# Kernel tuning notes

Hardware: AMD Instinct MI355X
Metric: run time of the kernel (lower is better)

Reference implementation:

```python
import jax, jax.numpy as jnp
import numpy as np

B, T, C, E = 2, 100, 80, 32
MH = MW = 64
IN_H = IN_W = 640.0
IOU_FACTOR, CLS_FACTOR, TOPK = 6.0, 0.5, 10
EPS = 1e-9


def get_anchors_and_scalers(fmaps, in_h, in_w):
    anchors, scalers = [], []
    for fh, fw in fmaps:
        stride = in_h / fh
        ys = (np.arange(fh) + 0.5) * stride
        xs = (np.arange(fw) + 0.5) * stride
        gy, gx = np.meshgrid(ys, xs, indexing='ij')
        anchors.append(np.stack([gx, gy], -1).reshape(-1, 2))
        scalers.append(np.full(fh * fw, stride))
    return (np.concatenate(anchors).astype(np.float32),
            np.concatenate(scalers).astype(np.float32))


def setup_inputs() -> dict:
    key = jax.random.key(0)
    ks = jax.random.split(key, 8)
    anchors_np, scalers_np = get_anchors_and_scalers([(80, 80), (40, 40), (20, 20)], IN_H, IN_W)
    anchors = jnp.asarray(anchors_np)
    scalers = jnp.asarray(scalers_np)
    A = anchors.shape[0]
    cls_logits = jax.random.normal(ks[0], (B, A, C), jnp.float32)
    wh = jax.random.uniform(ks[1], (B, A, 2), jnp.float32, 16.0, 160.0)
    ctr = anchors[None] + jax.random.normal(ks[2], (B, A, 2), jnp.float32) * 8.0
    pred_boxes = jnp.clip(jnp.concatenate([ctr - wh / 2, ctr + wh / 2], -1), 0.0, IN_W)
    mask_embs = jax.random.normal(ks[3], (B, A, E), jnp.float32)
    protos = jax.random.normal(ks[4], (B, MH, MW, E), jnp.float32)
    tl = jax.random.uniform(ks[5], (B, T, 2), jnp.float32, 0.0, 560.0)
    twh = jax.random.uniform(ks[6], (B, T, 2), jnp.float32, 30.0, 240.0)
    target_bbox = jnp.concatenate([tl, jnp.minimum(tl + twh, IN_W)], -1)
    target_cls = jax.random.randint(ks[7], (B, T), 0, C, jnp.int32)
    target_masks = (jax.random.uniform(jax.random.fold_in(key, 7), (B, MH, MW, T)) > 0.5).astype(jnp.float32)
    return {'cls_logits': cls_logits, 'pred_boxes': pred_boxes, 'mask_embs': mask_embs,
            'protos': protos, 'target_cls': target_cls, 'target_bbox': target_bbox,
            'target_masks': target_masks, 'anchors': anchors, 'scalers': scalers}


def _ciou_pairwise(gt, pr):
    # gt [B,T,4], pr [B,A,4] -> [B,T,A]
    g = gt[:, :, None, :]
    p = pr[:, None, :, :]
    ix1 = jnp.maximum(g[..., 0], p[..., 0]); iy1 = jnp.maximum(g[..., 1], p[..., 1])
    ix2 = jnp.minimum(g[..., 2], p[..., 2]); iy2 = jnp.minimum(g[..., 3], p[..., 3])
    inter = jnp.clip(ix2 - ix1, 0.0) * jnp.clip(iy2 - iy1, 0.0)
    wg = g[..., 2] - g[..., 0]; hg = g[..., 3] - g[..., 1]
    wp = p[..., 2] - p[..., 0]; hp = p[..., 3] - p[..., 1]
    union = wg * hg + wp * hp - inter + EPS
    iou = inter / union
    cw = jnp.maximum(g[..., 2], p[..., 2]) - jnp.minimum(g[..., 0], p[..., 0])
    ch = jnp.maximum(g[..., 3], p[..., 3]) - jnp.minimum(g[..., 1], p[..., 1])
    c2 = cw * cw + ch * ch + EPS
    rho2 = ((g[..., 0] + g[..., 2] - p[..., 0] - p[..., 2]) ** 2 +
            (g[..., 1] + g[..., 3] - p[..., 1] - p[..., 3]) ** 2) / 4.0
    v = (4.0 / (jnp.pi ** 2)) * (jnp.arctan(wg / (hg + EPS)) - jnp.arctan(wp / (hp + EPS))) ** 2
    alpha = jax.lax.stop_gradient(v / (1.0 - iou + v + EPS))
    return iou - rho2 / c2 - alpha * v


def _bbox_mask(boxes, mh, mw, in_h, in_w):
    # boxes [B,A,4] pixel xyxy -> [B,A,mh,mw] binary inside-box mask on mask grid
    sx, sy = mw / in_w, mh / in_h
    x1, y1, x2, y2 = boxes[..., 0] * sx, boxes[..., 1] * sy, boxes[..., 2] * sx, boxes[..., 3] * sy
    rows = jnp.arange(mh, dtype=boxes.dtype)
    cols = jnp.arange(mw, dtype=boxes.dtype)
    rm = (rows >= y1[..., None]) & (rows < y2[..., None])  # [B,A,mh]
    cm = (cols >= x1[..., None]) & (cols < x2[..., None])  # [B,A,mw]
    return (rm[..., :, None] & cm[..., None, :]).astype(boxes.dtype)


def _assign_and_build(cls_logits, pred_boxes, mask_embs, protos,
                      target_cls, target_bbox, target_masks, anchors, scalers):
    Bn, A, Cn = cls_logits.shape
    mh, mw = protos.shape[1], protos.shape[2]
    # --- task-aligned assigner ---
    lt, rb = target_bbox[:, :, None, :2], target_bbox[:, :, None, 2:]
    deltas = jnp.concatenate([anchors[None, None] - lt, rb - anchors[None, None]], -1)
    grid_mask = (jnp.min(deltas, -1) > 0).astype(cls_logits.dtype)  # [B,T,A]
    iou_mat = jnp.clip(_ciou_pairwise(target_bbox, pred_boxes), 0.0, 1.0)  # [B,T,A]
    cls_prob = jax.nn.sigmoid(cls_logits)  # [B,A,C]
    oh_t = jax.nn.one_hot(target_cls, Cn, dtype=cls_prob.dtype)  # [B,T,C]
    cls_mat = jnp.einsum('btc,bac->bta', oh_t, cls_prob)  # [B,T,A]
    tmat = grid_mask * (iou_mat ** IOU_FACTOR) * (cls_mat ** CLS_FACTOR)
    kth = jax.lax.top_k(tmat, TOPK)[0][..., -1:]  # [B,T,1]
    topk_targets = jnp.where((tmat >= kth) & (tmat > 0), tmat, 0.0)
    unique_idx = jnp.argmax(topk_targets, axis=1)  # [B,A] best GT per anchor
    valid = (jnp.sum(topk_targets, axis=1) > 0).astype(cls_logits.dtype)  # [B,A]
    align_bbox = jnp.take_along_axis(target_bbox, jnp.broadcast_to(unique_idx[..., None], (Bn, A, 4)), axis=1)
    align_cls_idx = jnp.take_along_axis(target_cls, unique_idx, axis=1)  # [B,A]
    max_target = jnp.max(tmat, axis=-1, keepdims=True)
    max_iou = jnp.max(iou_mat, axis=-1, keepdims=True)
    norm_term = tmat / (max_target + EPS) * max_iou  # [B,T,A]
    norm_g = jnp.take_along_axis(jnp.transpose(norm_term, (0, 2, 1)), unique_idx[..., None], axis=2)  # [B,A,1]
    align_cls = jax.nn.one_hot(align_cls_idx, Cn, dtype=cls_logits.dtype) * norm_g * valid[..., None]
    # --- loss-target assembly (compute_loss body) ---
    align_bbox_scaled = align_bbox / scalers[None, :, None]
    boxes_scaled = pred_boxes / scalers[None, :, None]
    box_target = jnp.concatenate([align_bbox_scaled, valid[..., None], align_cls], -1)
    box_mask = _bbox_mask(align_bbox, mh, mw, IN_H, IN_W)  # [B,A,mh,mw]
    valid_seg = box_mask * valid[..., None, None]
    seg_pred = jax.nn.sigmoid(jnp.einsum('bne,bhwe->bnhw', mask_embs, protos)) * valid_seg
    seg_pred = seg_pred.reshape(Bn, A, mh * mw)
    masks_t = jnp.transpose(target_masks, (0, 3, 1, 2))  # [B,T,mh,mw]
    idx4 = jnp.broadcast_to(unique_idx[..., None, None], (Bn, A, mh, mw))
    align_seg = (jnp.take_along_axis(masks_t, idx4, axis=1) * valid_seg).reshape(Bn, A, mh * mw)
    area = ((align_bbox[..., 2] - align_bbox[..., 0]) * (align_bbox[..., 3] - align_bbox[..., 1])
            / (IN_W * IN_H))
    seg_target = jnp.concatenate([area[..., None], valid[..., None], align_seg], -1)
    return jnp.concatenate([boxes_scaled, cls_logits, box_target, seg_pred, seg_target], -1)


def reference(cls_logits, pred_boxes, mask_embs, protos, target_cls, target_bbox,
              target_masks, anchors, scalers):
    return _assign_and_build(cls_logits, pred_boxes, mask_embs, protos,
                             target_cls, target_bbox, target_masks, anchors, scalers)
```

## Files before the change

kernel.cpp:

```cpp
#include <hip/hip_runtime.h>
#include <math.h>

#define A_TOT 8400
#define B_N   2
#define T_N   100
#define C_N   80
#define E_N   32
#define MH_N  64
#define MW_N  64
#define ROW_N 8363
#define NROWS (B_N*A_TOT)
#define EPSF  1e-9f
#define COMP_CAP 1536
#define NEGINF -1e30f

__device__ __forceinline__ float2 tmat_eval(
    float gx1, float gy1, float gx2, float gy2,
    float ax,  float ay,
    float px1, float py1, float px2, float py2,
    float cl, float atg, float atp) {
  float ix1 = fmaxf(gx1,px1), iy1 = fmaxf(gy1,py1);
  float ix2 = fminf(gx2,px2), iy2 = fminf(gy2,py2);
  float inter = fmaxf(ix2-ix1,0.f) * fmaxf(iy2-iy1,0.f);
  float wg = gx2-gx1, hg = gy2-gy1, wp = px2-px1, hp = py2-py1;
  float uni = wg*hg + wp*hp - inter + EPSF;
  float iou = inter / uni;
  float cw = fmaxf(gx2,px2) - fminf(gx1,px1);
  float ch = fmaxf(gy2,py2) - fminf(gy1,py1);
  float c2 = cw*cw + ch*ch + EPSF;
  float dx = gx1+gx2-px1-px2, dy = gy1+gy2-py1-py2;
  float rho2 = (dx*dx + dy*dy) * 0.25f;
  float da = atg - atp;
  float v  = 0.4052847345693511f * da * da;
  float alpha = v / (1.f - iou + v + EPSF);
  float ciou = iou - rho2/c2 - alpha*v;
  float iouc = fminf(fmaxf(ciou, 0.f), 1.f);

  float tm = 0.f;
  if (ax > gx1 && ay > gy1 && ax < gx2 && ay < gy2) {
    float cp = 1.f / (1.f + expf(-cl));
    float i2 = iouc * iouc;
    tm = i2*i2*i2 * sqrtf(cp);
  }
  return make_float2(tm, iouc);
}

__global__ __launch_bounds__(512) void k_score(
    const float* __restrict__ cls_logits, const float* __restrict__ pred_boxes,
    const float* __restrict__ target_bbox, const int* __restrict__ target_cls,
    const float* __restrict__ anchors,
    float* __restrict__ tmat,
    float* __restrict__ kth, float* __restrict__ maxt, float* __restrict__ maxiou) {
  int bt   = blockIdx.x;
  int b    = bt / T_N;
  int tid  = threadIdx.x;
  int lane = tid & 63, wid = tid >> 6;
  __shared__ float comp[COMP_CAP];
  __shared__ float redm[8], redi[8];
  __shared__ float wtop[8][10];
  __shared__ int   cnt;
  if (tid == 0) cnt = 0;
  __syncthreads();

  float4 g  = *(const float4*)(target_bbox + bt*4);
  int    tc = target_cls[bt];
  float atg = atanf((g.z - g.x) / ((g.w - g.y) + EPSF));
  float* trow = tmat + (size_t)bt * A_TOT;

  float lm = 0.f, li = 0.f;
  for (int a = tid; a < A_TOT; a += 512) {
    float ax = anchors[a*2+0], ay = anchors[a*2+1];
    float4 pb = *(const float4*)(pred_boxes + ((size_t)(b*A_TOT+a))*4);
    float cl = cls_logits[((size_t)(b*A_TOT+a))*C_N + tc];
    float atp = atanf((pb.z - pb.x) / ((pb.w - pb.y) + EPSF));
    float2 r = tmat_eval(g.x,g.y,g.z,g.w, ax,ay, pb.x,pb.y,pb.z,pb.w,
                         cl, atg, atp);
    trow[a] = r.x;
    li = fmaxf(li, r.y);
    if (r.x > 0.f) {
      lm = fmaxf(lm, r.x);
      comp[atomicAdd(&cnt, 1)] = r.x;
    }
  }
  #pragma unroll
  for (int off = 32; off; off >>= 1) {
    lm = fmaxf(lm, __shfl_xor(lm, off));
    li = fmaxf(li, __shfl_xor(li, off));
  }
  if (lane == 0) { redm[wid] = lm; redi[wid] = li; }
  __syncthreads();
  if (tid == 0) {
    float m = redm[0], mi = redi[0];
    #pragma unroll
    for (int w = 1; w < 8; w++) { m = fmaxf(m, redm[w]); mi = fmaxf(mi, redi[w]); }
    maxt[bt] = m; maxiou[bt] = mi;
  }
  int count = cnt;

  int base = wid*64 + lane;
  float e0 = (base        < count) ? comp[base]        : NEGINF;
  float e1 = (base + 512  < count) ? comp[base + 512]  : NEGINF;
  float e2 = (base + 1024 < count) ? comp[base + 1024] : NEGINF;
  float mytop = NEGINF;
  #pragma unroll
  for (int k = 0; k < 10; k++) {
    float bv = e0; int bs = 0;
    if (e1 > bv) { bv = e1; bs = 1; }
    if (e2 > bv) { bv = e2; bs = 2; }
    float v = bv; int id = (lane << 2) | bs;
    #pragma unroll
    for (int off = 32; off; off >>= 1) {
      float ov = __shfl_xor(v, off); int oid = __shfl_xor(id, off);
      if (ov > v || (ov == v && oid < id)) { v = ov; id = oid; }
    }
    if ((id >> 2) == lane) {
      int s = id & 3;
      if (s == 0) e0 = NEGINF; else if (s == 1) e1 = NEGINF; else e2 = NEGINF;
    }
    if (lane == k) mytop = v;
  }
  if (lane < 10) wtop[wid][lane] = mytop;
  __syncthreads();

  if (wid == 0) {
    int ia = lane, ib = 64 + lane;
    float f0 = wtop[ia/10][ia%10];
    float f1 = (ib < 80) ? wtop[ib/10][ib%10] : NEGINF;
    float cur = NEGINF;
    #pragma unroll
    for (int k = 0; k < 10; k++) {
      float bv = f0; int bs = 0;
      if (f1 > bv) { bv = f1; bs = 1; }
      float v = bv; int id = (lane << 1) | bs;
      #pragma unroll
      for (int off = 32; off; off >>= 1) {
        float ov = __shfl_xor(v, off); int oid = __shfl_xor(id, off);
        if (ov > v || (ov == v && oid < id)) { v = ov; id = oid; }
      }
      if ((id >> 1) == lane) { if ((id & 1) == 0) f0 = NEGINF; else f1 = NEGINF; }
      cur = v;
    }
    if (lane == 0) kth[bt] = fmaxf(cur, 0.f);
  }
}

__global__ __launch_bounds__(256) void k_sparse(
    const float* __restrict__ cls_logits, const float* __restrict__ pred_boxes,
    const float* __restrict__ mask_embs,  const float* __restrict__ protos,
    const float* __restrict__ t_masks,    const float* __restrict__ tmat,
    const float* __restrict__ kth, const float* __restrict__ maxt,
    const float* __restrict__ maxiou, const float* __restrict__ target_bbox,
    const int* __restrict__ target_cls, const float* __restrict__ scalers,
    float* __restrict__ out) {
  unsigned row = blockIdx.x;
  int b   = row >= (unsigned)A_TOT;
  int a   = (int)row - b*A_TOT;
  int tid = threadIdx.x;
  __shared__ float sv[128];
  __shared__ int   st[128];
  __shared__ float semb[E_N];
  __shared__ float ctx[10];

  if (tid < 128) {
    float v = 0.f; int tt = 0x7fff;
    if (tid < T_N) {
      int bt = b*T_N + tid;
      float tv = tmat[(size_t)bt*A_TOT + a];
      if (tv > 0.f && tv >= kth[bt]) { v = tv; tt = tid; }
    }
    sv[tid] = v; st[tid] = tt;
  }
  if (tid < E_N) semb[tid] = mask_embs[(size_t)row*E_N + tid];
  __syncthreads();
  if (tid < 64) {
    float v1 = sv[tid];    int t1 = st[tid];
    float v2 = sv[tid+64]; int t2 = st[tid+64];
    if (v2 > v1 || (v2 == v1 && t2 < t1)) { v1 = v2; t1 = t2; }
    #pragma unroll
    for (int off = 32; off; off >>= 1) {
      float ov = __shfl_xor(v1, off); int ot = __shfl_xor(t1, off);
      if (ov > v1 || (ov == v1 && ot < t1)) { v1 = ov; t1 = ot; }
    }
    if (tid == 0) {
      int anyv = v1 > 0.f;
      int u = anyv ? t1 : 0;
      int bu = b*T_N + u;
      float4 tb = *(const float4*)(target_bbox + bu*4);
      float ng = anyv ? v1 / (maxt[bu] + EPSF) * maxiou[bu] : 0.f;
      ctx[0]=tb.x; ctx[1]=tb.y; ctx[2]=tb.z; ctx[3]=tb.w;
      ctx[4]= anyv ? 1.f : 0.f; ctx[5]=ng; ctx[6]=scalers[a];
      ctx[7]= (tb.z-tb.x)*(tb.w-tb.y)/(640.f*640.f);
      ctx[8]=__int_as_float(u); ctx[9]=__int_as_float(target_cls[bu]);
    }
  }
  __syncthreads();
  float tb0=ctx[0], tb1=ctx[1], tb2=ctx[2], tb3=ctx[3];
  float vld=ctx[4], ng=ctx[5], s=ctx[6], area=ctx[7];
  int   u  =__float_as_int(ctx[8]), ct=__float_as_int(ctx[9]);
  bool valid = vld > 0.5f;
  size_t base = (size_t)row * ROW_N;

  if (tid < 92) {
    if (tid < 4)        out[base + tid] = pred_boxes[(size_t)row*4 + tid] / s;
    else if (tid < 84)  out[base + tid] = cls_logits[(size_t)row*C_N + (tid-4)];
    else if (tid < 88) {
      float t = (tid==84)?tb0:((tid==85)?tb1:((tid==86)?tb2:tb3));
      out[base + tid] = t / s;
    }
    else if (tid == 88) out[base + 88] = vld;
    else if (tid == 89) { if (valid) out[base + 89 + ct] = ng; }
    else if (tid == 90) out[base + 4265] = area;
    else                out[base + 4266] = vld;
  }
  if (!valid) return;

  float x1s=tb0*0.1f, y1s=tb1*0.1f, x2s=tb2*0.1f, y2s=tb3*0.1f;
  for (int p = tid; p < MH_N*MW_N; p += 256) {
    int h = p >> 6, w = p & 63;
    float fh = (float)h, fw = (float)w;
    if (fh >= y1s && fh < y2s && fw >= x1s && fw < x2s) {
      const float* pr = protos + ((size_t)((b*MH_N + h)*MW_N + w)) * E_N;
      float acc = 0.f;
      #pragma unroll
      for (int e = 0; e < E_N; e++) acc += semb[e] * pr[e];
      out[base + 169  + p] = 1.f / (1.f + expf(-acc));
      out[base + 4267 + p] = t_masks[((size_t)((b*MH_N + h)*MW_N + w)) * T_N + u];
    }
  }
}

extern "C" void kernel_launch(void* const* d_in, const int* in_sizes, int n_in,
                              void* d_out, int out_size, void* d_ws, size_t ws_size,
                              hipStream_t stream) {
  const float* cls_logits   = (const float*)d_in[0];
  const float* pred_boxes   = (const float*)d_in[1];
  const float* mask_embs    = (const float*)d_in[2];
  const float* protos       = (const float*)d_in[3];
  const int*   target_cls   = (const int*)  d_in[4];
  const float* target_bbox  = (const float*)d_in[5];
  const float* target_masks = (const float*)d_in[6];
  const float* anchors      = (const float*)d_in[7];
  const float* scalers      = (const float*)d_in[8];
  float* out = (float*)d_out;

  float* ws     = (float*)d_ws;
  float* tmat   = ws;
  float* kth    = tmat + (size_t)B_N*T_N*A_TOT;
  float* maxt   = kth + B_N*T_N;
  float* maxiou = maxt + B_N*T_N;

  hipMemsetAsync(out, 0, (size_t)out_size * sizeof(float), stream);
  k_score<<<B_N*T_N, 512, 0, stream>>>(cls_logits, pred_boxes, target_bbox,
                                       target_cls, anchors, tmat, kth, maxt, maxiou);
  k_sparse<<<NROWS, 256, 0, stream>>>(cls_logits, pred_boxes, mask_embs, protos,
                                      target_masks, tmat, kth, maxt, maxiou,
                                      target_bbox, target_cls, scalers, out);
}
```

Before: 178.4 us.

## Fuse output zeroing into score kernel, transpose tmat, persistent output kernel

Replaces the separate memset with extra blocks in the score kernel that zero the output using vector stores, so zeroing runs alongside the score computation. The score matrix is stored anchor-major so the per-row gather in the output kernel becomes contiguous. The output kernel becomes a grid-stride loop over rows with a fixed grid, and the mask loop walks only the box's cell range instead of testing all 4096 cells. The trade-off is strided writes to the score matrix and extra syncs per row.

```diff
diff --git a/kernel.cpp b/kernel.cpp
--- a/kernel.cpp
+++ b/kernel.cpp
@@ -13,6 +13,11 @@
 #define EPSF  1e-9f
 #define COMP_CAP 1536
 #define NEGINF -1e30f
+#define GMAIN 1024
+#define NZOFF 200
+#define GOUT  2048
+
+typedef float vfloat4 __attribute__((ext_vector_type(4)));
 
 __device__ __forceinline__ float2 tmat_eval(
     float gx1, float gy1, float gx2, float gy2,
@@ -45,14 +50,31 @@
   return make_float2(tm, iouc);
 }
 
-__global__ __launch_bounds__(512) void k_score(
+__global__ __launch_bounds__(512) void k_main(
     const float* __restrict__ cls_logits, const float* __restrict__ pred_boxes,
     const float* __restrict__ target_bbox, const int* __restrict__ target_cls,
     const float* __restrict__ anchors,
-    float* __restrict__ tmat,
-    float* __restrict__ kth, float* __restrict__ maxt, float* __restrict__ maxiou) {
+    float* __restrict__ tmatT,
+    float* __restrict__ kth, float* __restrict__ maxt, float* __restrict__ maxiou,
+    float* __restrict__ out) {
+  if (blockIdx.x >= NZOFF) {
+    const unsigned total4 = (unsigned)NROWS * ROW_N / 4u;
+    unsigned stride = (GMAIN - NZOFF) * 512u;
+    unsigned c = (blockIdx.x - NZOFF) * 512u + threadIdx.x;
+    vfloat4 z = (vfloat4)(0.f);
+    for (; c + 3u*stride < total4; c += 4u*stride) {
+      *(vfloat4*)(out + (size_t)4u*c)               = z;
+      *(vfloat4*)(out + (size_t)4u*(c +    stride)) = z;
+      *(vfloat4*)(out + (size_t)4u*(c + 2u*stride)) = z;
+      *(vfloat4*)(out + (size_t)4u*(c + 3u*stride)) = z;
+    }
+    for (; c < total4; c += stride)
+      *(vfloat4*)(out + (size_t)4u*c) = z;
+    return;
+  }
   int bt   = blockIdx.x;
   int b    = bt / T_N;
+  int t    = bt - b*T_N;
   int tid  = threadIdx.x;
   int lane = tid & 63, wid = tid >> 6;
   __shared__ float comp[COMP_CAP];
@@ -65,7 +87,6 @@
   float4 g  = *(const float4*)(target_bbox + bt*4);
   int    tc = target_cls[bt];
   float atg = atanf((g.z - g.x) / ((g.w - g.y) + EPSF));
-  float* trow = tmat + (size_t)bt * A_TOT;
 
   float lm = 0.f, li = 0.f;
   for (int a = tid; a < A_TOT; a += 512) {
@@ -75,7 +96,7 @@
     float atp = atanf((pb.z - pb.x) / ((pb.w - pb.y) + EPSF));
     float2 r = tmat_eval(g.x,g.y,g.z,g.w, ax,ay, pb.x,pb.y,pb.z,pb.w,
                          cl, atg, atp);
-    trow[a] = r.x;
+    tmatT[((size_t)b*A_TOT + a)*T_N + t] = r.x;
     li = fmaxf(li, r.y);
     if (r.x > 0.f) {
       lm = fmaxf(lm, r.x);
@@ -144,88 +165,93 @@
   }
 }
 
-__global__ __launch_bounds__(256) void k_sparse(
+__global__ __launch_bounds__(256) void k_out(
     const float* __restrict__ cls_logits, const float* __restrict__ pred_boxes,
     const float* __restrict__ mask_embs,  const float* __restrict__ protos,
-    const float* __restrict__ t_masks,    const float* __restrict__ tmat,
+    const float* __restrict__ t_masks,    const float* __restrict__ tmatT,
     const float* __restrict__ kth, const float* __restrict__ maxt,
     const float* __restrict__ maxiou, const float* __restrict__ target_bbox,
     const int* __restrict__ target_cls, const float* __restrict__ scalers,
     float* __restrict__ out) {
-  unsigned row = blockIdx.x;
-  int b   = row >= (unsigned)A_TOT;
-  int a   = (int)row - b*A_TOT;
   int tid = threadIdx.x;
   __shared__ float sv[128];
   __shared__ int   st[128];
   __shared__ float semb[E_N];
   __shared__ float ctx[10];
 
-  if (tid < 128) {
-    float v = 0.f; int tt = 0x7fff;
-    if (tid < T_N) {
-      int bt = b*T_N + tid;
-      float tv = tmat[(size_t)bt*A_TOT + a];
-      if (tv > 0.f && tv >= kth[bt]) { v = tv; tt = tid; }
-    }
-    sv[tid] = v; st[tid] = tt;
-  }
-  if (tid < E_N) semb[tid] = mask_embs[(size_t)row*E_N + tid];
-  __syncthreads();
-  if (tid < 64) {
-    float v1 = sv[tid];    int t1 = st[tid];
-    float v2 = sv[tid+64]; int t2 = st[tid+64];
-    if (v2 > v1 || (v2 == v1 && t2 < t1)) { v1 = v2; t1 = t2; }
-    #pragma unroll
-    for (int off = 32; off; off >>= 1) {
-      float ov = __shfl_xor(v1, off); int ot = __shfl_xor(t1, off);
-      if (ov > v1 || (ov == v1 && ot < t1)) { v1 = ov; t1 = ot; }
-    }
-    if (tid == 0) {
-      int anyv = v1 > 0.f;
-      int u = anyv ? t1 : 0;
-      int bu = b*T_N + u;
-      float4 tb = *(const float4*)(target_bbox + bu*4);
-      float ng = anyv ? v1 / (maxt[bu] + EPSF) * maxiou[bu] : 0.f;
-      ctx[0]=tb.x; ctx[1]=tb.y; ctx[2]=tb.z; ctx[3]=tb.w;
-      ctx[4]= anyv ? 1.f : 0.f; ctx[5]=ng; ctx[6]=scalers[a];
-      ctx[7]= (tb.z-tb.x)*(tb.w-tb.y)/(640.f*640.f);
-      ctx[8]=__int_as_float(u); ctx[9]=__int_as_float(target_cls[bu]);
-    }
-  }
-  __syncthreads();
-  float tb0=ctx[0], tb1=ctx[1], tb2=ctx[2], tb3=ctx[3];
-  float vld=ctx[4], ng=ctx[5], s=ctx[6], area=ctx[7];
-  int   u  =__float_as_int(ctx[8]), ct=__float_as_int(ctx[9]);
-  bool valid = vld > 0.5f;
-  size_t base = (size_t)row * ROW_N;
-
-  if (tid < 92) {
-    if (tid < 4)        out[base + tid] = pred_boxes[(size_t)row*4 + tid] / s;
-    else if (tid < 84)  out[base + tid] = cls_logits[(size_t)row*C_N + (tid-4)];
-    else if (tid < 88) {
-      float t = (tid==84)?tb0:((tid==85)?tb1:((tid==86)?tb2:tb3));
-      out[base + tid] = t / s;
-    }
-    else if (tid == 88) out[base + 88] = vld;
-    else if (tid == 89) { if (valid) out[base + 89 + ct] = ng; }
-    else if (tid == 90) out[base + 4265] = area;
-    else                out[base + 4266] = vld;
-  }
-  if (!valid) return;
-
-  float x1s=tb0*0.1f, y1s=tb1*0.1f, x2s=tb2*0.1f, y2s=tb3*0.1f;
-  for (int p = tid; p < MH_N*MW_N; p += 256) {
-    int h = p >> 6, w = p & 63;
-    float fh = (float)h, fw = (float)w;
-    if (fh >= y1s && fh < y2s && fw >= x1s && fw < x2s) {
-      const float* pr = protos + ((size_t)((b*MH_N + h)*MW_N + w)) * E_N;
-      float acc = 0.f;
+  for (unsigned row = blockIdx.x; row < (unsigned)NROWS; row += GOUT) {
+    int b = row >= (unsigned)A_TOT;
+    int a = (int)row - b*A_TOT;
+
+    if (tid < 128) {
+      float v = 0.f; int tt = 0x7fff;
+      if (tid < T_N) {
+        float tv = tmatT[(size_t)row*T_N + tid];
+        if (tv > 0.f && tv >= kth[b*T_N + tid]) { v = tv; tt = tid; }
+      }
+      sv[tid] = v; st[tid] = tt;
+    }
+    if (tid < E_N) semb[tid] = mask_embs[(size_t)row*E_N + tid];
+    __syncthreads();
+    if (tid < 64) {
+      float v1 = sv[tid];    int t1 = st[tid];
+      float v2 = sv[tid+64]; int t2 = st[tid+64];
+      if (v2 > v1 || (v2 == v1 && t2 < t1)) { v1 = v2; t1 = t2; }
       #pragma unroll
-      for (int e = 0; e < E_N; e++) acc += semb[e] * pr[e];
-      out[base + 169  + p] = 1.f / (1.f + expf(-acc));
-      out[base + 4267 + p] = t_masks[((size_t)((b*MH_N + h)*MW_N + w)) * T_N + u];
-    }
+      for (int off = 32; off; off >>= 1) {
+        float ov = __shfl_xor(v1, off); int ot = __shfl_xor(t1, off);
+        if (ov > v1 || (ov == v1 && ot < t1)) { v1 = ov; t1 = ot; }
+      }
+      if (tid == 0) {
+        int anyv = v1 > 0.f;
+        int u = anyv ? t1 : 0;
+        int bu = b*T_N + u;
+        float4 tb = *(const float4*)(target_bbox + bu*4);
+        float ng = anyv ? v1 / (maxt[bu] + EPSF) * maxiou[bu] : 0.f;
+        ctx[0]=tb.x; ctx[1]=tb.y; ctx[2]=tb.z; ctx[3]=tb.w;
+        ctx[4]= anyv ? 1.f : 0.f; ctx[5]=ng; ctx[6]=scalers[a];
+        ctx[7]= (tb.z-tb.x)*(tb.w-tb.y)/(640.f*640.f);
+        ctx[8]=__int_as_float(u); ctx[9]=__int_as_float(target_cls[bu]);
+      }
+    }
+    __syncthreads();
+    float tb0=ctx[0], tb1=ctx[1], tb2=ctx[2], tb3=ctx[3];
+    float vld=ctx[4], ng=ctx[5], s=ctx[6], area=ctx[7];
+    int   u  =__float_as_int(ctx[8]), ct=__float_as_int(ctx[9]);
+    bool valid = vld > 0.5f;
+    size_t base = (size_t)row * ROW_N;
+
+    if (tid < 92) {
+      if (tid < 4)        out[base + tid] = pred_boxes[(size_t)row*4 + tid] / s;
+      else if (tid < 84)  out[base + tid] = cls_logits[(size_t)row*C_N + (tid-4)];
+      else if (tid < 88) {
+        float t = (tid==84)?tb0:((tid==85)?tb1:((tid==86)?tb2:tb3));
+        out[base + tid] = t / s;
+      }
+      else if (tid == 88) out[base + 88] = vld;
+      else if (tid == 89) { if (valid) out[base + 89 + ct] = ng; }
+      else if (tid == 90) out[base + 4265] = area;
+      else                out[base + 4266] = vld;
+    }
+
+    if (valid) {
+      float x1s=tb0*0.1f, y1s=tb1*0.1f, x2s=tb2*0.1f, y2s=tb3*0.1f;
+      int hlo = max(0, (int)ceilf(y1s)), hhi = min(MH_N, (int)ceilf(y2s));
+      int wlo = max(0, (int)ceilf(x1s)), whi = min(MW_N, (int)ceilf(x2s));
+      int nw = whi - wlo, nh = hhi - hlo;
+      int ncell = (nw > 0 && nh > 0) ? nw * nh : 0;
+      for (int i = tid; i < ncell; i += 256) {
+        int h = hlo + i / nw, w = wlo + i % nw;
+        const float* pr = protos + ((size_t)((b*MH_N + h)*MW_N + w)) * E_N;
+        float acc = 0.f;
+        #pragma unroll
+        for (int e = 0; e < E_N; e++) acc += semb[e] * pr[e];
+        int p = (h << 6) | w;
+        out[base + 169  + p] = 1.f / (1.f + expf(-acc));
+        out[base + 4267 + p] = t_masks[((size_t)((b*MH_N + h)*MW_N + w)) * T_N + u];
+      }
+    }
+    __syncthreads();
   }
 }
 
@@ -244,15 +270,15 @@
   float* out = (float*)d_out;
 
   float* ws     = (float*)d_ws;
-  float* tmat   = ws;
-  float* kth    = tmat + (size_t)B_N*T_N*A_TOT;
+  float* tmatT  = ws;
+  float* kth    = tmatT + (size_t)NROWS*T_N;
   float* maxt   = kth + B_N*T_N;
   float* maxiou = maxt + B_N*T_N;
 
-  hipMemsetAsync(out, 0, (size_t)out_size * sizeof(float), stream);
-  k_score<<<B_N*T_N, 512, 0, stream>>>(cls_logits, pred_boxes, target_bbox,
-                                       target_cls, anchors, tmat, kth, maxt, maxiou);
-  k_sparse<<<NROWS, 256, 0, stream>>>(cls_logits, pred_boxes, mask_embs, protos,
-                                      target_masks, tmat, kth, maxt, maxiou,
-                                      target_bbox, target_cls, scalers, out);
-}
+  k_main<<<GMAIN, 512, 0, stream>>>(cls_logits, pred_boxes, target_bbox,
+                                    target_cls, anchors, tmatT, kth, maxt,
+                                    maxiou, out);
+  k_out<<<GOUT, 256, 0, stream>>>(cls_logits, pred_boxes, mask_embs, protos,
+                                  target_masks, tmatT, kth, maxt, maxiou,
+                                  target_bbox, target_cls, scalers, out);
+}
```

Measured after the change: 182.9 us. 2.5% more time.
